# Kernel tuning notes

Measured on AMD Instinct MI355X. Metric: run time of the kernel, lower is better.

Reference implementation:

```python
import jax, jax.numpy as jnp
import numpy as np

H = 16        # num_heads
D = 128       # head_dim = hidden_size // num_heads
HID = 2048    # hidden_size
BLOCK = 64    # moba_chunk_size
TOPK = 8      # moba_topk


def setup_inputs() -> dict:
    key = jax.random.key(0)
    ks = jax.random.split(key, 5)
    B, S = 1, 2048
    hidden_states = jax.random.normal(ks[0], (B, S, HID), dtype=jnp.float32)
    scale = HID ** -0.5
    Wq = jax.random.normal(ks[1], (HID, H * D), dtype=jnp.float32) * scale
    Wk = jax.random.normal(ks[2], (HID, H * D), dtype=jnp.float32) * scale
    Wv = jax.random.normal(ks[3], (HID, H * D), dtype=jnp.float32) * scale
    Wo = jax.random.normal(ks[4], (H * D, HID), dtype=jnp.float32) * scale
    return {"hidden_states": hidden_states, "Wq": Wq, "Wk": Wk, "Wv": Wv, "Wo": Wo}


def _moba_forward(hidden_states, Wq, Wk, Wv, Wo):
    B, S, _ = hidden_states.shape
    nb = S // BLOCK
    INF = jnp.float32(jnp.inf)

    q = (hidden_states @ Wq).reshape(B, S, H, D)
    k = (hidden_states @ Wk).reshape(B, S, H, D)
    v = (hidden_states @ Wv).reshape(B, S, H, D)

    # MoBA gating: mean-pooled key per block -> [B, nb, H, D]
    kg = k.reshape(B, nb, BLOCK, H, D).mean(axis=2)
    gate = jnp.einsum('bshd,bnhd->bhsn', q, kg)  # [B,H,S,nb]

    pos = jnp.arange(S)
    qb = pos // BLOCK                 # query's own block
    blk = jnp.arange(nb)
    is_self = qb[:, None] == blk[None, :]                      # self block always selected
    not_past = pos[:, None] < (blk[None, :] + 1) * BLOCK       # blocks not fully in the past
    gate = jnp.where(is_self, INF, jnp.where(not_past, -INF, gate))

    kk = min(TOPK, nb)
    topv, topi = jax.lax.top_k(gate, kk)                       # [B,H,S,kk]
    thresh = topv.min(axis=-1, keepdims=True)
    idx_mask = (topi[..., None] == blk).any(axis=-2)           # [B,H,S,nb]
    need = (gate >= thresh) & idx_mask
    gate_bias = jnp.where(need, 0.0, -INF)                     # additive block mask

    sm_scale = D ** -0.5
    qk = jnp.einsum('bshd,bthd->bhst', q, k) * sm_scale        # [B,H,S,S]
    qk = qk.reshape(B, H, S, nb, BLOCK) + gate_bias[..., None]
    qk = qk.reshape(B, H, S, S)
    causal = pos[:, None] >= pos[None, :]
    qk = jnp.where(causal, qk, -INF)

    p = jax.nn.softmax(qk, axis=-1)
    o = jnp.einsum('bhst,bthd->bshd', p, v).reshape(B, S, H * D)
    return o @ Wo


def reference(hidden_states, Wq, Wk, Wv, Wo):
    # Returns (output, attentions=None, past_key_values=None) in the original;
    # only the output tensor matters for correctness.
    return _moba_forward(hidden_states, Wq, Wk, Wv, Wo)
```

## Files before the change

### kernel.cpp

```cpp
#include <hip/hip_runtime.h>
#include <hip/hip_bf16.h>
#include <stdint.h>
#include <stddef.h>


using bh = __bf16;
typedef __bf16 bhx8 __attribute__((ext_vector_type(8)));
typedef __bf16 bhx4 __attribute__((ext_vector_type(4)));
typedef float  f32x4 __attribute__((ext_vector_type(4)));

#define SEQ   2048
#define HIDN  2048
#define NHEAD 16
#define HDIM  128
#define NBLK  32
#define BLKSZ 64
#define NQKV  6144
#define NGATE 512
#define LDC   136
#define PSTRIDE ((size_t)SEQ * NGATE)

#define GLDS16(gsrc, ldst)                                                     \
  __builtin_amdgcn_global_load_lds(                                            \
      (const __attribute__((address_space(1))) uint32_t*)(gsrc),               \
      (__attribute__((address_space(3))) uint32_t*)(ldst), 16, 0, 0)

__global__ __launch_bounds__(256) void split_f32(const float* __restrict__ in,
                                                 bh* __restrict__ hi, bh* __restrict__ lo, int n) {
  int i = (blockIdx.x * 256 + threadIdx.x) * 4;
  if (i >= n) return;
  float4 v = *(const float4*)(in + i);
  bhx4 h4, l4;
  float vv[4] = {v.x, v.y, v.z, v.w};
#pragma unroll
  for (int e = 0; e < 4; e++) {
    bh h = (bh)vv[e];
    h4[e] = h;
    l4[e] = (bh)(vv[e] - (float)h);
  }
  *(bhx4*)(hi + i) = h4;
  *(bhx4*)(lo + i) = l4;
}

__global__ __launch_bounds__(256) void transpose_cast4(const float* __restrict__ Wq,
                                                       const float* __restrict__ Wk,
                                                       const float* __restrict__ Wv,
                                                       const float* __restrict__ Wo,
                                                       bh* __restrict__ wqkvT, bh* __restrict__ woT) {
  __shared__ float tile[32][33];
  const int z = blockIdx.z;
  const float* in = (z == 0) ? Wq : (z == 1) ? Wk : (z == 2) ? Wv : Wo;
  bh* out = (z < 3) ? (wqkvT + (size_t)z * HIDN * HIDN) : woT;
  int tx = threadIdx.x, ty = threadIdx.y;
  int c0 = blockIdx.x * 32, r0 = blockIdx.y * 32;
#pragma unroll
  for (int i = 0; i < 4; i++)
    tile[ty + i * 8][tx] = in[(size_t)(r0 + ty + i * 8) * HIDN + c0 + tx];
  __syncthreads();
#pragma unroll
  for (int i = 0; i < 4; i++)
    out[(size_t)(c0 + ty + i * 8) * HIDN + r0 + tx] = (bh)tile[tx][ty + i * 8];
}

#define GEMM_STAGE_TILE(SRC, r0_, ldsbase)                                       \
  {                                                                              \
    _Pragma("unroll")                                                            \
    for (int it_ = 0; it_ < 4; it_++) {                                          \
      int idx_ = it_ * 256 + t;                                                  \
      int row_ = idx_ >> 3, x_ = (idx_ & 7) << 4;                                \
      GLDS16((const char*)(SRC) + (size_t)(r0_ + row_) * strideB + kbyte +       \
                 (x_ ^ ((row_ & 7) << 4)),                                       \
             (char*)(ldsbase) + ((idx_ >> 6) << 10));                            \
    }                                                                            \
  }

__global__ __launch_bounds__(256) void qkvkg(const bh* __restrict__ A, const bh* __restrict__ BT,
                                             bh* __restrict__ Cb,
                                             const float* __restrict__ hsm,
                                             const float* __restrict__ Wk,
                                             float* __restrict__ part) {
  __shared__ __align__(16) char smraw[128 * LDC * 2];
  const int t = threadIdx.x;

  if (blockIdx.x < 768) {
    bh* smem = (bh*)smraw;
    bh* As = smem;
    bh* Bs = smem + 128 * 64;
    const int L = t & 63, w = t >> 6;
    const int wm = w & 1, wn = w >> 1;
    const int quad = L >> 4, lo = L & 15;
    const int m0 = (blockIdx.x / 48) * 128, n0 = (blockIdx.x % 48) * 128;
    const size_t strideB = (size_t)HIDN * 2;

    f32x4 acc[4][4];
#pragma unroll
    for (int i = 0; i < 4; i++)
#pragma unroll
      for (int j = 0; j < 4; j++) acc[i][j] = (f32x4){0.f, 0.f, 0.f, 0.f};

    for (int k0 = 0; k0 < HIDN; k0 += 64) {
      const size_t kbyte = (size_t)k0 * 2;
      GEMM_STAGE_TILE(A, m0, As);
      GEMM_STAGE_TILE(BT, n0, Bs);
      __syncthreads();
#pragma unroll
      for (int ks = 0; ks < 2; ks++) {
        bhx8 af[4], bf_[4];
#pragma unroll
        for (int i = 0; i < 4; i++) {
          const int row = wm * 64 + i * 16 + lo;
          af[i] = *(const bhx8*)((const char*)As + row * 128 +
                                 ((ks * 64 + quad * 16) ^ ((row & 7) << 4)));
        }
#pragma unroll
        for (int j = 0; j < 4; j++) {
          const int row = wn * 64 + j * 16 + lo;
          bf_[j] = *(const bhx8*)((const char*)Bs + row * 128 +
                                  ((ks * 64 + quad * 16) ^ ((row & 7) << 4)));
        }
#pragma unroll
        for (int i = 0; i < 4; i++)
#pragma unroll
          for (int j = 0; j < 4; j++)
            acc[i][j] = __builtin_amdgcn_mfma_f32_16x16x32_bf16(af[i], bf_[j], acc[i][j], 0, 0, 0);
      }
      __syncthreads();
    }

    bh* Cs = smem;
#pragma unroll
    for (int i = 0; i < 4; i++)
#pragma unroll
      for (int j = 0; j < 4; j++)
#pragma unroll
        for (int r = 0; r < 4; r++)
          Cs[(wm * 64 + i * 16 + quad * 4 + r) * LDC + wn * 64 + j * 16 + lo] = (bh)acc[i][j][r];
    __syncthreads();
#pragma unroll
    for (int it = 0; it < 8; it++) {
      int idx = it * 256 + t;
      int row = idx >> 4, cg = idx & 15;
      *(uint4*)(Cb + (size_t)(m0 + row) * NQKV + n0 + cg * 8) = *(const uint4*)&Cs[row * LDC + cg * 8];
    }
  } else {
    float (*hl)[32] = (float (*)[32])smraw;
    const int b2 = blockIdx.x - 768;
    const int c = (b2 & 7) * 256 + t;
    const int ky = b2 >> 3;
    const int k0 = ky * 32;
    for (int i = t; i < 32 * 32; i += 256)
      hl[i >> 5][i & 31] = hsm[(size_t)(i >> 5) * HIDN + k0 + (i & 31)];
    __syncthreads();
    float acc[32];
#pragma unroll
    for (int n = 0; n < 32; n++) acc[n] = 0.f;
#pragma unroll 2
    for (int k4 = 0; k4 < 8; k4++) {
      float w0 = Wk[(size_t)(k0 + k4 * 4 + 0) * HIDN + c];
      float w1 = Wk[(size_t)(k0 + k4 * 4 + 1) * HIDN + c];
      float w2 = Wk[(size_t)(k0 + k4 * 4 + 2) * HIDN + c];
      float w3 = Wk[(size_t)(k0 + k4 * 4 + 3) * HIDN + c];
#pragma unroll
      for (int n = 0; n < 32; n++) {
        float4 hv = *(const float4*)&hl[n][k4 * 4];
        acc[n] += hv.x * w0 + hv.y * w1 + hv.z * w2 + hv.w * w3;
      }
    }
#pragma unroll
    for (int n = 0; n < 32; n++)
      part[((size_t)ky * 32 + n) * HIDN + c] = acc[n];
  }
}

__global__ __launch_bounds__(256) void gemm_bt128f(const bh* __restrict__ A, const bh* __restrict__ BT,
                                                   float* __restrict__ Cf, int M, int N, int K) {
  __shared__ __align__(16) bh smem[2 * 128 * 64];
  bh* As = smem;
  bh* Bs = smem + 128 * 64;
  const int t = threadIdx.x;
  const int L = t & 63, w = t >> 6;
  const int wm = w & 1, wn = w >> 1;
  const int quad = L >> 4, lo = L & 15;
  const int m0 = blockIdx.y * 128, n0 = blockIdx.x * 128;
  const size_t strideB = (size_t)K * 2;

  f32x4 acc[4][4];
#pragma unroll
  for (int i = 0; i < 4; i++)
#pragma unroll
    for (int j = 0; j < 4; j++) acc[i][j] = (f32x4){0.f, 0.f, 0.f, 0.f};

  for (int k0 = 0; k0 < K; k0 += 64) {
    const size_t kbyte = (size_t)k0 * 2;
    GEMM_STAGE_TILE(A, m0, As);
    GEMM_STAGE_TILE(BT, n0, Bs);
    __syncthreads();
#pragma unroll
    for (int ks = 0; ks < 2; ks++) {
      bhx8 af[4], bf_[4];
#pragma unroll
      for (int i = 0; i < 4; i++) {
        const int row = wm * 64 + i * 16 + lo;
        af[i] = *(const bhx8*)((const char*)As + row * 128 +
                               ((ks * 64 + quad * 16) ^ ((row & 7) << 4)));
      }
#pragma unroll
      for (int j = 0; j < 4; j++) {
        const int row = wn * 64 + j * 16 + lo;
        bf_[j] = *(const bhx8*)((const char*)Bs + row * 128 +
                                ((ks * 64 + quad * 16) ^ ((row & 7) << 4)));
      }
#pragma unroll
      for (int i = 0; i < 4; i++)
#pragma unroll
        for (int j = 0; j < 4; j++)
          acc[i][j] = __builtin_amdgcn_mfma_f32_16x16x32_bf16(af[i], bf_[j], acc[i][j], 0, 0, 0);
    }
    __syncthreads();
  }

#pragma unroll
  for (int i = 0; i < 4; i++)
#pragma unroll
    for (int j = 0; j < 4; j++)
#pragma unroll
      for (int r = 0; r < 4; r++) {
        int row = m0 + wm * 64 + i * 16 + quad * 4 + r;
        int col = n0 + wn * 64 + j * 16 + lo;
        Cf[(size_t)row * N + col] = acc[i][j][r];
      }
}

__global__ __launch_bounds__(256) void gemm_gate_split(const bh* __restrict__ hs_hi,
                                                       const bh* __restrict__ hs_lo,
                                                       const bh* __restrict__ wg_hi,
                                                       const bh* __restrict__ wg_lo,
                                                       float* __restrict__ part) {
  __shared__ __align__(16) bh smem[2 * 128 * 64];
  bh* As = smem;
  bh* Bs = smem + 128 * 64;
  const int t = threadIdx.x;
  const int L = t & 63, w = t >> 6;
  const int wm = w & 1, wn = w >> 1;
  const int quad = L >> 4, lo = L & 15;
  const int m0 = blockIdx.y * 128, n0 = blockIdx.x * 128;
  const int z = blockIdx.z;
  const bh* Ap = ((z >> 1) == 1) ? hs_lo : hs_hi;
  const bh* Bp = ((z >> 1) == 2) ? wg_lo : wg_hi;
  const int kb = (z & 1) * 1024;
  const size_t strideB = (size_t)HIDN * 2;

  f32x4 acc[4][4];
#pragma unroll
  for (int i = 0; i < 4; i++)
#pragma unroll
    for (int j = 0; j < 4; j++) acc[i][j] = (f32x4){0.f, 0.f, 0.f, 0.f};

  for (int k0 = 0; k0 < 1024; k0 += 64) {
    const size_t kbyte = (size_t)(kb + k0) * 2;
    GEMM_STAGE_TILE(Ap, m0, As);
    GEMM_STAGE_TILE(Bp, n0, Bs);
    __syncthreads();
#pragma unroll
    for (int ks = 0; ks < 2; ks++) {
      bhx8 af[4], bf_[4];
#pragma unroll
      for (int i = 0; i < 4; i++) {
        const int row = wm * 64 + i * 16 + lo;
        af[i] = *(const bhx8*)((const char*)As + row * 128 +
                               ((ks * 64 + quad * 16) ^ ((row & 7) << 4)));
      }
#pragma unroll
      for (int j = 0; j < 4; j++) {
        const int row = wn * 64 + j * 16 + lo;
        bf_[j] = *(const bhx8*)((const char*)Bs + row * 128 +
                                ((ks * 64 + quad * 16) ^ ((row & 7) << 4)));
      }
#pragma unroll
      for (int i = 0; i < 4; i++)
#pragma unroll
        for (int j = 0; j < 4; j++)
          acc[i][j] = __builtin_amdgcn_mfma_f32_16x16x32_bf16(af[i], bf_[j], acc[i][j], 0, 0, 0);
    }
    __syncthreads();
  }

#pragma unroll
  for (int i = 0; i < 4; i++)
#pragma unroll
    for (int j = 0; j < 4; j++)
#pragma unroll
      for (int r = 0; r < 4; r++) {
        int row = m0 + wm * 64 + i * 16 + quad * 4 + r;
        int col = n0 + wn * 64 + j * 16 + lo;
        part[(size_t)z * PSTRIDE + (size_t)row * NGATE + col] = acc[i][j][r];
      }
}

__global__ __launch_bounds__(256) void hsmean_k(const float* __restrict__ hs, float* __restrict__ hsm) {
  int idx = blockIdx.x * 256 + threadIdx.x;
  int n = idx >> 11, c = idx & 2047;
  const float* p = hs + (size_t)(n * BLKSZ) * HIDN + c;
  float s = 0.f;
#pragma unroll 8
  for (int r = 0; r < BLKSZ; r++) s += p[(size_t)r * HIDN];
  hsm[idx] = s * (1.0f / 64.0f);
}

__global__ __launch_bounds__(256) void kg_reduce64(const float* __restrict__ part, float* __restrict__ kg) {
  int idx = blockIdx.x * 256 + threadIdx.x;
  float s = 0.f;
#pragma unroll
  for (int kc = 0; kc < 64; kc++) s += part[(size_t)kc * 65536 + idx];
  kg[idx] = s;
}

__global__ __launch_bounds__(256) void wg_k(const float* __restrict__ Wq, const float* __restrict__ kg,
                                            float* __restrict__ wg) {
  __shared__ float kl[32][128];
  int h = blockIdx.y;
  int r = blockIdx.x * 256 + threadIdx.x;
  for (int i = threadIdx.x; i < 32 * 128; i += 256)
    kl[i >> 7][i & 127] = kg[(size_t)(i >> 7) * HIDN + h * HDIM + (i & 127)];
  __syncthreads();
  float acc[32];
#pragma unroll
  for (int n = 0; n < 32; n++) acc[n] = 0.f;
  const float4* wrow = (const float4*)(Wq + (size_t)r * HIDN + h * HDIM);
  for (int d4 = 0; d4 < 32; d4++) {
    float4 w = wrow[d4];
#pragma unroll
    for (int n = 0; n < 32; n++) {
      float4 kv = *(const float4*)&kl[n][d4 * 4];
      acc[n] += w.x * kv.x + w.y * kv.y + w.z * kv.z + w.w * kv.w;
    }
  }
#pragma unroll
  for (int n = 0; n < 32; n++)
    wg[(size_t)(h * 32 + n) * HIDN + r] = acc[n];
}

__global__ __launch_bounds__(256) void gate_topk(const float* __restrict__ part,
                                                 unsigned* __restrict__ bsel) {
  int w = threadIdx.x >> 6, L = threadIdx.x & 63;
  int p = blockIdx.x * 4 + w;
  int h = p >> 11, s = p & 2047;
  int qb = s >> 6;
  int n = L;
  float g = -1e30f;
  if (n == qb) g = 1e30f;
  else if (n < qb) {
    size_t off = (size_t)s * NGATE + h * 32 + n;
    g = part[off] + part[off + PSTRIDE] + part[off + 2 * PSTRIDE] +
        part[off + 3 * PSTRIDE] + part[off + 4 * PSTRIDE] + part[off + 5 * PSTRIDE];
  }
  int rank = 0;
#pragma unroll
  for (int j = 0; j < 32; j++) {
    float gj = __shfl(g, j, 64);
    if (gj > g || (gj == g && j < n)) rank++;
  }
  bool sel = (n <= qb) && (n < 32) && (rank < 8);
  unsigned long long bm = __ballot(sel);
  if (L == 0) bsel[p] = (unsigned)(bm & 0xffffffffull);
}

__global__ __launch_bounds__(256) void vtrans(const bh* __restrict__ qkv, bh* __restrict__ vt) {
  __shared__ float tile[32][33];
  int tx = threadIdx.x, ty = threadIdx.y;
  int s0 = blockIdx.x * 32, d0 = blockIdx.y * 32, h = blockIdx.z;
#pragma unroll
  for (int i = 0; i < 4; i++)
    tile[ty + i * 8][tx] = (float)qkv[(size_t)(s0 + ty + i * 8) * NQKV + 2 * HIDN + h * HDIM + d0 + tx];
  __syncthreads();
#pragma unroll
  for (int i = 0; i < 4; i++)
    vt[((size_t)h * HDIM + d0 + ty + i * 8) * SEQ + s0 + tx] = (bh)tile[tx][ty + i * 8];
}

__global__ __launch_bounds__(256) void attn(const bh* __restrict__ qkv, const bh* __restrict__ vt,
                                            const unsigned* __restrict__ bsel, bh* __restrict__ obuf) {
  __shared__ __align__(16) bh Ksm[2][64 * 128];
  __shared__ __align__(16) bh Vsm[2][128 * 64];
  __shared__ __align__(16) bh PLb[4][16 * 72];
  __shared__ unsigned ublk;
  const int t = threadIdx.x;
  const int w = t >> 6, L = t & 63;
  const int quad = L >> 4, lo = L & 15;
  const int bid = blockIdx.x;
  const int jj = bid >> 3;
  const int h = ((bid & 7) << 1) | (jj & 1);
  const int qb = (jj < 32) ? (31 - (jj >> 1)) : ((jj - 32) >> 1);
  const int s0 = qb * 64 + w * 16;

  unsigned bs[4];
#pragma unroll
  for (int r = 0; r < 4; r++) bs[r] = bsel[h * SEQ + s0 + quad * 4 + r];
  unsigned uni = bs[0] | bs[1] | bs[2] | bs[3];
  uni |= (unsigned)__shfl_xor((int)uni, 16);
  uni |= (unsigned)__shfl_xor((int)uni, 32);
  const unsigned uniw = uni;
  if (t == 0) ublk = 0;
  __syncthreads();
  if (L == 0) atomicOr(&ublk, uni);
  __syncthreads();
  const unsigned un = ublk;

  bhx8 aq[4];
  const bh* qrow = qkv + (size_t)(s0 + lo) * NQKV + h * HDIM;
#pragma unroll
  for (int ks = 0; ks < 4; ks++) aq[ks] = *(const bhx8*)(qrow + ks * 32 + quad * 8);

  f32x4 oacc[8];
#pragma unroll
  for (int j = 0; j < 8; j++) oacc[j] = (f32x4){0.f, 0.f, 0.f, 0.f};
  f32x4 lacc = (f32x4){0.f, 0.f, 0.f, 0.f};
  float mi[4] = {-1e30f, -1e30f, -1e30f, -1e30f};

  bhx8 ones8;
#pragma unroll
  for (int e = 0; e < 8; e++) ones8[e] = (bh)1.0f;

  const float scale = 0.08838834764831845f;

  auto stageKV = [&](int b, int n) {
    const char* ksrc = (const char*)(qkv + (size_t)(n * BLKSZ) * NQKV + HIDN + h * HDIM);
    const char* vsrc = (const char*)(vt + ((size_t)h * HDIM) * SEQ + n * BLKSZ);
    char* kb = (char*)&Ksm[b][0];
    char* vb = (char*)&Vsm[b][0];
#pragma unroll
    for (int it = 0; it < 4; it++) {
      int idx = it * 256 + t;
      int row = idx >> 4, x = (idx & 15) << 4;
      GLDS16(ksrc + (size_t)row * (NQKV * 2) + (x ^ ((row & 7) << 4)),
             kb + ((idx >> 6) << 10));
    }
#pragma unroll
    for (int it = 0; it < 4; it++) {
      int idx = it * 256 + t;
      int row = idx >> 3, x = (idx & 7) << 4;
      GLDS16(vsrc + (size_t)row * (SEQ * 2) + (x ^ ((row & 7) << 4)),
             vb + ((idx >> 6) << 10));
    }
  };

  unsigned rem = un;
  int ncur = (int)__builtin_ctz(rem);
  rem &= rem - 1;
  stageKV(0, ncur);
  int cur = 0;

  while (true) {
    int nnext = -1;
    if (rem) { nnext = (int)__builtin_ctz(rem); rem &= rem - 1; }
    if (nnext >= 0) {
      stageKV(cur ^ 1, nnext);
      asm volatile("s_waitcnt vmcnt(8)" ::: "memory");
    } else {
      asm volatile("s_waitcnt vmcnt(0)" ::: "memory");
    }
    __builtin_amdgcn_s_barrier();

    if ((uniw >> ncur) & 1) {
      const char* Kc = (const char*)&Ksm[cur][0];
      const char* Vc = (const char*)&Vsm[cur][0];
      const bool self = (ncur == qb);

      f32x4 sc[4];
      __builtin_amdgcn_s_setprio(1);
#pragma unroll
      for (int nt = 0; nt < 4; nt++) {
        f32x4 s4 = (f32x4){0.f, 0.f, 0.f, 0.f};
#pragma unroll
        for (int ks = 0; ks < 4; ks++) {
          const int row = nt * 16 + lo;
          bhx8 bk = *(const bhx8*)(Kc + row * 256 + ((ks * 64 + quad * 16) ^ ((row & 7) << 4)));
          s4 = __builtin_amdgcn_mfma_f32_16x16x32_bf16(aq[ks], bk, s4, 0, 0, 0);
        }
        sc[nt] = s4;
      }
      __builtin_amdgcn_s_setprio(0);

      if (self) {
#pragma unroll
        for (int nt = 0; nt < 4; nt++)
#pragma unroll
          for (int r = 0; r < 4; r++) {
            float v = sc[nt][r] * scale;
            int kpos = ncur * BLKSZ + nt * 16 + lo;
            int qpos = s0 + quad * 4 + r;
            bool ok = ((bs[r] >> ncur) & 1) && (kpos <= qpos);
            sc[nt][r] = ok ? v : -1e30f;
          }
      } else {
        float bias[4];
#pragma unroll
        for (int r = 0; r < 4; r++)
          bias[r] = ((bs[r] >> ncur) & 1) ? 0.f : -1e30f;
#pragma unroll
        for (int nt = 0; nt < 4; nt++)
#pragma unroll
          for (int r = 0; r < 4; r++)
            sc[nt][r] = sc[nt][r] * scale + bias[r];
      }
      float rm[4];
#pragma unroll
      for (int r = 0; r < 4; r++)
        rm[r] = fmaxf(fmaxf(sc[0][r], sc[1][r]), fmaxf(sc[2][r], sc[3][r]));
#pragma unroll
      for (int off = 1; off < 16; off <<= 1)
#pragma unroll
        for (int r = 0; r < 4; r++) rm[r] = fmaxf(rm[r], __shfl_xor(rm[r], off));

      bool exceed = (rm[0] > mi[0] + 8.f) || (rm[1] > mi[1] + 8.f) ||
                    (rm[2] > mi[2] + 8.f) || (rm[3] > mi[3] + 8.f);
      if (__any(exceed)) {
        float alpha[4];
#pragma unroll
        for (int r = 0; r < 4; r++) {
          float nm = fmaxf(mi[r], rm[r]);
          alpha[r] = __expf(mi[r] - nm);
          mi[r] = nm;
        }
#pragma unroll
        for (int j = 0; j < 8; j++)
#pragma unroll
          for (int r = 0; r < 4; r++) oacc[j][r] *= alpha[r];
#pragma unroll
        for (int r = 0; r < 4; r++) lacc[r] *= alpha[r];
      }

#pragma unroll
      for (int nt = 0; nt < 4; nt++)
#pragma unroll
        for (int r = 0; r < 4; r++) {
          float pv = __expf(sc[nt][r] - mi[r]);
          PLb[w][(quad * 4 + r) * 72 + nt * 16 + lo] = (bh)pv;
        }

      __builtin_amdgcn_s_setprio(1);
#pragma unroll
      for (int kk = 0; kk < 2; kk++) {
        bhx8 pa = *(const bhx8*)&PLb[w][lo * 72 + kk * 32 + quad * 8];
        lacc = __builtin_amdgcn_mfma_f32_16x16x32_bf16(pa, ones8, lacc, 0, 0, 0);
#pragma unroll
        for (int j = 0; j < 8; j++) {
          const int row = j * 16 + lo;
          bhx8 vv = *(const bhx8*)(Vc + row * 128 + ((kk * 64 + quad * 16) ^ ((row & 7) << 4)));
          oacc[j] = __builtin_amdgcn_mfma_f32_16x16x32_bf16(pa, vv, oacc[j], 0, 0, 0);
        }
      }
      __builtin_amdgcn_s_setprio(0);
    }

    __builtin_amdgcn_s_barrier();
    if (nnext < 0) break;
    ncur = nnext;
    cur ^= 1;
  }

#pragma unroll
  for (int j = 0; j < 8; j++)
#pragma unroll
    for (int r = 0; r < 4; r++) {
      int row = s0 + quad * 4 + r;
      int col = h * HDIM + j * 16 + lo;
      obuf[(size_t)row * HIDN + col] = (bh)(oacc[j][r] / lacc[r]);
    }
}

extern "C" void kernel_launch(void* const* d_in, const int* in_sizes, int n_in,
                              void* d_out, int out_size, void* d_ws, size_t ws_size,
                              hipStream_t stream) {
  const float* hs = (const float*)d_in[0];
  const float* Wq = (const float*)d_in[1];
  const float* Wk = (const float*)d_in[2];
  const float* Wv = (const float*)d_in[3];
  const float* Wo = (const float*)d_in[4];

  char* ws = (char*)d_ws;
  bh* hs_hi = (bh*)ws;            ws += (size_t)SEQ * HIDN * 2;
  bh* hs_lo = (bh*)ws;            ws += (size_t)SEQ * HIDN * 2;
  bh* wqkvT = (bh*)ws;            ws += (size_t)NQKV * HIDN * 2;
  bh* woT = (bh*)ws;              ws += (size_t)HIDN * HIDN * 2;
  bh* qkv = (bh*)ws;              ws += (size_t)SEQ * NQKV * 2;
  bh* vt = (bh*)ws;               ws += (size_t)NHEAD * HDIM * SEQ * 2;
  bh* obuf = (bh*)ws;             ws += (size_t)SEQ * HIDN * 2;
  float* hsm = (float*)ws;        ws += (size_t)NBLK * HIDN * 4;
  float* kg = (float*)ws;         ws += (size_t)NBLK * HIDN * 4;
  float* wg = (float*)ws;         ws += (size_t)NGATE * HIDN * 4;
  bh* wg_hi = (bh*)ws;            ws += (size_t)NGATE * HIDN * 2;
  bh* wg_lo = (bh*)ws;            ws += (size_t)NGATE * HIDN * 2;
  unsigned* bsel = (unsigned*)ws; ws += (size_t)NHEAD * SEQ * 4;
  float* kg_part = (float*)vt;
  float* gpart = (float*)wqkvT;

  split_f32<<<(SEQ * HIDN) / 1024, 256, 0, stream>>>(hs, hs_hi, hs_lo, SEQ * HIDN);
  transpose_cast4<<<dim3(64, 64, 4), dim3(32, 8), 0, stream>>>(Wq, Wk, Wv, Wo, wqkvT, woT);
  hsmean_k<<<(NBLK * HIDN) / 256, 256, 0, stream>>>(hs, hsm);

  qkvkg<<<768 + 512, 256, 0, stream>>>(hs_hi, wqkvT, qkv, hsm, Wk, kg_part);

  kg_reduce64<<<(NBLK * HIDN) / 256, 256, 0, stream>>>(kg_part, kg);
  wg_k<<<dim3(8, NHEAD), 256, 0, stream>>>(Wq, kg, wg);
  split_f32<<<(NGATE * HIDN) / 1024, 256, 0, stream>>>(wg, wg_hi, wg_lo, NGATE * HIDN);
  gemm_gate_split<<<dim3(NGATE / 128, SEQ / 128, 6), 256, 0, stream>>>(hs_hi, hs_lo, wg_hi, wg_lo, gpart);
  gate_topk<<<(NHEAD * SEQ) / 4, 256, 0, stream>>>(gpart, bsel);

  vtrans<<<dim3(SEQ / 32, HDIM / 32, NHEAD), dim3(32, 8), 0, stream>>>(qkv, vt);
  attn<<<dim3(NBLK * NHEAD), 256, 0, stream>>>(qkv, vt, bsel, obuf);

  gemm_bt128f<<<dim3(HIDN / 128, SEQ / 128), 256, 0, stream>>>(obuf, woT, (float*)d_out, SEQ, HIDN, HIDN);
}
```

Baseline: 421.1 us.

## Fuse wg split into wg_k, rebalance gate GEMM split-K, single-buffer attention KV

wg_k now stages Wq tiles through shared memory transposed and writes the hi/lo bf16 split directly, which drops the fp32 wg buffer and the separate split_f32 launch. The gate GEMM splits its virtual K range into 8 chunks of 768 instead of 6 of 1024, so the grid has more blocks. The extra partials go to a second buffer that aliases vt, and gate_topk sums all eight. The attention kernel drops double-buffered KV staging with asynchronous prefetch in favour of a single buffer with full syncs. That halves its LDS use but removes the overlap between loads and compute.

```diff
diff --git a/kernel.cpp b/kernel.cpp
--- a/kernel.cpp
+++ b/kernel.cpp
@@ -235,7 +235,8 @@
                                                        const bh* __restrict__ hs_lo,
                                                        const bh* __restrict__ wg_hi,
                                                        const bh* __restrict__ wg_lo,
-                                                       float* __restrict__ part) {
+                                                       float* __restrict__ part6,
+                                                       float* __restrict__ part2) {
   __shared__ __align__(16) bh smem[2 * 128 * 64];
   bh* As = smem;
   bh* Bs = smem + 128 * 64;
@@ -245,9 +246,6 @@
   const int quad = L >> 4, lo = L & 15;
   const int m0 = blockIdx.y * 128, n0 = blockIdx.x * 128;
   const int z = blockIdx.z;
-  const bh* Ap = ((z >> 1) == 1) ? hs_lo : hs_hi;
-  const bh* Bp = ((z >> 1) == 2) ? wg_lo : wg_hi;
-  const int kb = (z & 1) * 1024;
   const size_t strideB = (size_t)HIDN * 2;
 
   f32x4 acc[4][4];
@@ -256,8 +254,12 @@
 #pragma unroll
     for (int j = 0; j < 4; j++) acc[i][j] = (f32x4){0.f, 0.f, 0.f, 0.f};
 
-  for (int k0 = 0; k0 < 1024; k0 += 64) {
-    const size_t kbyte = (size_t)(kb + k0) * 2;
+  for (int k0 = 0; k0 < 768; k0 += 64) {
+    const int vk = z * 768 + k0;
+    const int ph = vk >> 11;
+    const bh* Ap = (ph == 1) ? hs_lo : hs_hi;
+    const bh* Bp = (ph == 2) ? wg_lo : wg_hi;
+    const size_t kbyte = (size_t)(vk & 2047) * 2;
     GEMM_STAGE_TILE(Ap, m0, As);
     GEMM_STAGE_TILE(Bp, n0, Bs);
     __syncthreads();
@@ -285,6 +287,7 @@
     __syncthreads();
   }
 
+  float* outp = (z < 6) ? (part6 + (size_t)z * PSTRIDE) : (part2 + (size_t)(z - 6) * PSTRIDE);
 #pragma unroll
   for (int i = 0; i < 4; i++)
 #pragma unroll
@@ -293,7 +296,7 @@
       for (int r = 0; r < 4; r++) {
         int row = m0 + wm * 64 + i * 16 + quad * 4 + r;
         int col = n0 + wn * 64 + j * 16 + lo;
-        part[(size_t)z * PSTRIDE + (size_t)row * NGATE + col] = acc[i][j][r];
+        outp[(size_t)row * NGATE + col] = acc[i][j][r];
       }
 }
 
@@ -316,31 +319,48 @@
 }
 
 __global__ __launch_bounds__(256) void wg_k(const float* __restrict__ Wq, const float* __restrict__ kg,
-                                            float* __restrict__ wg) {
-  __shared__ float kl[32][128];
-  int h = blockIdx.y;
-  int r = blockIdx.x * 256 + threadIdx.x;
-  for (int i = threadIdx.x; i < 32 * 128; i += 256)
+                                            bh* __restrict__ wg_hi, bh* __restrict__ wg_lo) {
+  __shared__ float wst[128][65];
+  __shared__ float kl[32][129];
+  const int h = blockIdx.y;
+  const int r0 = blockIdx.x * 256;
+  const int t = threadIdx.x;
+  const int rloc = t & 63, ng = t >> 6;
+
+  for (int i = t; i < 32 * 128; i += 256)
     kl[i >> 7][i & 127] = kg[(size_t)(i >> 7) * HIDN + h * HDIM + (i & 127)];
-  __syncthreads();
-  float acc[32];
-#pragma unroll
-  for (int n = 0; n < 32; n++) acc[n] = 0.f;
-  const float4* wrow = (const float4*)(Wq + (size_t)r * HIDN + h * HDIM);
-  for (int d4 = 0; d4 < 32; d4++) {
-    float4 w = wrow[d4];
-#pragma unroll
-    for (int n = 0; n < 32; n++) {
-      float4 kv = *(const float4*)&kl[n][d4 * 4];
-      acc[n] += w.x * kv.x + w.y * kv.y + w.z * kv.z + w.w * kv.w;
-    }
-  }
-#pragma unroll
-  for (int n = 0; n < 32; n++)
-    wg[(size_t)(h * 32 + n) * HIDN + r] = acc[n];
-}
-
-__global__ __launch_bounds__(256) void gate_topk(const float* __restrict__ part,
+
+#pragma unroll
+  for (int rt = 0; rt < 4; rt++) {
+    __syncthreads();
+    for (int i = t; i < 64 * 128; i += 256) {
+      int row = i >> 7, col = i & 127;
+      wst[col][row] = Wq[(size_t)(r0 + rt * 64 + row) * HIDN + h * HDIM + col];
+    }
+    __syncthreads();
+    float acc8[8];
+#pragma unroll
+    for (int nn = 0; nn < 8; nn++) acc8[nn] = 0.f;
+    for (int d = 0; d < 128; d++) {
+      float wv = wst[d][rloc];
+#pragma unroll
+      for (int nn = 0; nn < 8; nn++)
+        acc8[nn] += wv * kl[ng * 8 + nn][d];
+    }
+#pragma unroll
+    for (int nn = 0; nn < 8; nn++) {
+      int n = ng * 8 + nn;
+      float v = acc8[nn];
+      bh hi = (bh)v;
+      size_t off = (size_t)(h * 32 + n) * HIDN + r0 + rt * 64 + rloc;
+      wg_hi[off] = hi;
+      wg_lo[off] = (bh)(v - (float)hi);
+    }
+  }
+}
+
+__global__ __launch_bounds__(256) void gate_topk(const float* __restrict__ part6,
+                                                 const float* __restrict__ part2,
                                                  unsigned* __restrict__ bsel) {
   int w = threadIdx.x >> 6, L = threadIdx.x & 63;
   int p = blockIdx.x * 4 + w;
@@ -351,8 +371,9 @@
   if (n == qb) g = 1e30f;
   else if (n < qb) {
     size_t off = (size_t)s * NGATE + h * 32 + n;
-    g = part[off] + part[off + PSTRIDE] + part[off + 2 * PSTRIDE] +
-        part[off + 3 * PSTRIDE] + part[off + 4 * PSTRIDE] + part[off + 5 * PSTRIDE];
+    g = part6[off] + part6[off + PSTRIDE] + part6[off + 2 * PSTRIDE] +
+        part6[off + 3 * PSTRIDE] + part6[off + 4 * PSTRIDE] + part6[off + 5 * PSTRIDE] +
+        part2[off] + part2[off + PSTRIDE];
   }
   int rank = 0;
 #pragma unroll
@@ -380,8 +401,8 @@
 
 __global__ __launch_bounds__(256) void attn(const bh* __restrict__ qkv, const bh* __restrict__ vt,
                                             const unsigned* __restrict__ bsel, bh* __restrict__ obuf) {
-  __shared__ __align__(16) bh Ksm[2][64 * 128];
-  __shared__ __align__(16) bh Vsm[2][128 * 64];
+  __shared__ __align__(16) bh Ksm[64 * 128];
+  __shared__ __align__(16) bh Vsm[128 * 64];
   __shared__ __align__(16) bh PLb[4][16 * 72];
   __shared__ unsigned ublk;
   const int t = threadIdx.x;
@@ -423,47 +444,34 @@
 
   const float scale = 0.08838834764831845f;
 
-  auto stageKV = [&](int b, int n) {
-    const char* ksrc = (const char*)(qkv + (size_t)(n * BLKSZ) * NQKV + HIDN + h * HDIM);
-    const char* vsrc = (const char*)(vt + ((size_t)h * HDIM) * SEQ + n * BLKSZ);
-    char* kb = (char*)&Ksm[b][0];
-    char* vb = (char*)&Vsm[b][0];
-#pragma unroll
-    for (int it = 0; it < 4; it++) {
-      int idx = it * 256 + t;
-      int row = idx >> 4, x = (idx & 15) << 4;
-      GLDS16(ksrc + (size_t)row * (NQKV * 2) + (x ^ ((row & 7) << 4)),
-             kb + ((idx >> 6) << 10));
-    }
-#pragma unroll
-    for (int it = 0; it < 4; it++) {
-      int idx = it * 256 + t;
-      int row = idx >> 3, x = (idx & 7) << 4;
-      GLDS16(vsrc + (size_t)row * (SEQ * 2) + (x ^ ((row & 7) << 4)),
-             vb + ((idx >> 6) << 10));
-    }
-  };
-
   unsigned rem = un;
-  int ncur = (int)__builtin_ctz(rem);
-  rem &= rem - 1;
-  stageKV(0, ncur);
-  int cur = 0;
-
-  while (true) {
-    int nnext = -1;
-    if (rem) { nnext = (int)__builtin_ctz(rem); rem &= rem - 1; }
-    if (nnext >= 0) {
-      stageKV(cur ^ 1, nnext);
-      asm volatile("s_waitcnt vmcnt(8)" ::: "memory");
-    } else {
-      asm volatile("s_waitcnt vmcnt(0)" ::: "memory");
-    }
-    __builtin_amdgcn_s_barrier();
+  while (rem) {
+    const int ncur = (int)__builtin_ctz(rem);
+    rem &= rem - 1;
+
+    {
+      const char* ksrc = (const char*)(qkv + (size_t)(ncur * BLKSZ) * NQKV + HIDN + h * HDIM);
+      const char* vsrc = (const char*)(vt + ((size_t)h * HDIM) * SEQ + ncur * BLKSZ);
+#pragma unroll
+      for (int it = 0; it < 4; it++) {
+        int idx = it * 256 + t;
+        int row = idx >> 4, x = (idx & 15) << 4;
+        GLDS16(ksrc + (size_t)row * (NQKV * 2) + (x ^ ((row & 7) << 4)),
+               (char*)Ksm + ((idx >> 6) << 10));
+      }
+#pragma unroll
+      for (int it = 0; it < 4; it++) {
+        int idx = it * 256 + t;
+        int row = idx >> 3, x = (idx & 7) << 4;
+        GLDS16(vsrc + (size_t)row * (SEQ * 2) + (x ^ ((row & 7) << 4)),
+               (char*)Vsm + ((idx >> 6) << 10));
+      }
+    }
+    __syncthreads();
 
     if ((uniw >> ncur) & 1) {
-      const char* Kc = (const char*)&Ksm[cur][0];
-      const char* Vc = (const char*)&Vsm[cur][0];
+      const char* Kc = (const char*)Ksm;
+      const char* Vc = (const char*)Vsm;
       const bool self = (ncur == qb);
 
       f32x4 sc[4];
@@ -553,10 +561,7 @@
       __builtin_amdgcn_s_setprio(0);
     }
 
-    __builtin_amdgcn_s_barrier();
-    if (nnext < 0) break;
-    ncur = nnext;
-    cur ^= 1;
+    __syncthreads();
   }
 
 #pragma unroll
@@ -588,12 +593,12 @@
   bh* obuf = (bh*)ws;             ws += (size_t)SEQ * HIDN * 2;
   float* hsm = (float*)ws;        ws += (size_t)NBLK * HIDN * 4;
   float* kg = (float*)ws;         ws += (size_t)NBLK * HIDN * 4;
-  float* wg = (float*)ws;         ws += (size_t)NGATE * HIDN * 4;
   bh* wg_hi = (bh*)ws;            ws += (size_t)NGATE * HIDN * 2;
   bh* wg_lo = (bh*)ws;            ws += (size_t)NGATE * HIDN * 2;
   unsigned* bsel = (unsigned*)ws; ws += (size_t)NHEAD * SEQ * 4;
   float* kg_part = (float*)vt;
-  float* gpart = (float*)wqkvT;
+  float* gpart6 = (float*)wqkvT;
+  float* gpart2 = (float*)vt;
 
   split_f32<<<(SEQ * HIDN) / 1024, 256, 0, stream>>>(hs, hs_hi, hs_lo, SEQ * HIDN);
   transpose_cast4<<<dim3(64, 64, 4), dim3(32, 8), 0, stream>>>(Wq, Wk, Wv, Wo, wqkvT, woT);
@@ -602,10 +607,10 @@
   qkvkg<<<768 + 512, 256, 0, stream>>>(hs_hi, wqkvT, qkv, hsm, Wk, kg_part);
 
   kg_reduce64<<<(NBLK * HIDN) / 256, 256, 0, stream>>>(kg_part, kg);
-  wg_k<<<dim3(8, NHEAD), 256, 0, stream>>>(Wq, kg, wg);
-  split_f32<<<(NGATE * HIDN) / 1024, 256, 0, stream>>>(wg, wg_hi, wg_lo, NGATE * HIDN);
-  gemm_gate_split<<<dim3(NGATE / 128, SEQ / 128, 6), 256, 0, stream>>>(hs_hi, hs_lo, wg_hi, wg_lo, gpart);
-  gate_topk<<<(NHEAD * SEQ) / 4, 256, 0, stream>>>(gpart, bsel);
+  wg_k<<<dim3(8, NHEAD), 256, 0, stream>>>(Wq, kg, wg_hi, wg_lo);
+  gemm_gate_split<<<dim3(NGATE / 128, SEQ / 128, 8), 256, 0, stream>>>(
+      hs_hi, hs_lo, wg_hi, wg_lo, gpart6, gpart2);
+  gate_topk<<<(NHEAD * SEQ) / 4, 256, 0, stream>>>(gpart6, gpart2, bsel);
 
   vtrans<<<dim3(SEQ / 32, HDIM / 32, NHEAD), dim3(32, 8), 0, stream>>>(qkv, vt);
   attn<<<dim3(NBLK * NHEAD), 256, 0, stream>>>(qkv, vt, bsel, obuf);
```

Result: no change. 413.2 us (-1.9%).
